# Optimization experiments

Hardware: AMD Instinct MI355X
Metric: run time of the kernel (lower is better)

## Reference

```python
import jax, jax.numpy as jnp
import numpy as np

C = 768; NH = 12; HD = 64; WS = 14; VPT = 10; H0 = 64; B = 8
SCALE = HD ** -0.5


def layernorm(x, w, b, eps=1e-5):
    m = x.mean(-1, keepdims=True)
    v = x.var(-1, keepdims=True)
    return (x - m) / jnp.sqrt(v + eps) * w + b


def setup_inputs() -> dict:
    key = jax.random.key(0)
    ks = jax.random.split(key, 8)
    def rn(k, shape, s=0.02):
        return jax.random.normal(k, shape, jnp.float32) * s
    L = VPT + H0 * H0
    return {
        "x": jax.random.normal(ks[0], (B, L, C), jnp.float32),
        "ln1_w": jnp.ones((C,), jnp.float32),
        "ln1_b": jnp.zeros((C,), jnp.float32),
        "qkv_w": rn(ks[1], (3 * C, C)),
        "qkv_b": jnp.zeros((3 * C,), jnp.float32),
        "proj_w": rn(ks[2], (C, C)),
        "proj_b": jnp.zeros((C,), jnp.float32),
        "rel_pos_h": rn(ks[3], (2 * WS - 1, HD)),
        "rel_pos_w": rn(ks[4], (2 * WS - 1, HD)),
        "ln2_w": jnp.ones((C,), jnp.float32),
        "ln2_b": jnp.zeros((C,), jnp.float32),
        "mlp_w1": rn(ks[5], (4 * C, C)),
        "mlp_b1": jnp.zeros((4 * C,), jnp.float32),
        "mlp_w2": rn(ks[6], (C, 4 * C)),
        "mlp_b2": jnp.zeros((C,), jnp.float32),
        "H": H0,
        "W": H0,
    }


def reference(x, ln1_w, ln1_b, qkv_w, qkv_b, proj_w, proj_b, rel_pos_h, rel_pos_w,
              ln2_w, ln2_b, mlp_w1, mlp_b1, mlp_w2, mlp_b2, H, W):
    B_, L, C_ = x.shape
    shortcut = x
    xn = layernorm(x, ln1_w, ln1_b)

    # --- window partition (SAM style, pad bottom/right) ---
    prompt = xn[:, :VPT]                           # (B, VPT, C)
    sp = xn[:, VPT:].reshape(B_, H, W, C_)
    pad_h = (WS - H % WS) % WS
    pad_w = (WS - W % WS) % WS
    Hp, Wp = H + pad_h, W + pad_w
    sp = jnp.pad(sp, ((0, 0), (0, pad_h), (0, pad_w), (0, 0)))
    nh, nw = Hp // WS, Wp // WS
    win = sp.reshape(B_, nh, WS, nw, WS, C_).transpose(0, 1, 3, 2, 4, 5)
    win = win.reshape(-1, WS * WS, C_)             # (B*nwin, WS*WS, C), batch-major
    nwin = nh * nw
    # faithful to original: prompts broadcast window-major, windows are batch-major
    pr = jnp.broadcast_to(prompt[None], (nwin, B_, VPT, C_)).reshape(-1, VPT, C_)
    tok = jnp.concatenate([pr, win], axis=1)       # (Bw, Lw, C)
    Bw, Lw, _ = tok.shape

    # --- attention with decomposed rel-pos ---
    qkv = tok @ qkv_w.T + qkv_b
    qkv = qkv.reshape(Bw, Lw, 3, NH, HD).transpose(2, 0, 3, 1, 4).reshape(3, Bw * NH, Lw, HD)
    q, k, v = qkv[0], qkv[1], qkv[2]
    attn = (q * SCALE) @ k.transpose(0, 2, 1)      # (Bw*NH, Lw, Lw)

    coords = jnp.arange(WS)[:, None] - jnp.arange(WS)[None, :] + (WS - 1)
    Rh = rel_pos_h[coords]                         # (WS, WS, HD)
    Rw = rel_pos_w[coords]
    rq = q[:, VPT:].reshape(Bw * NH, WS, WS, HD)
    rel_h = jnp.einsum('bhwc,hkc->bhwk', rq, Rh)
    rel_w = jnp.einsum('bhwc,wkc->bhwk', rq, Rw)
    ori = attn[:, VPT:, VPT:].reshape(-1, WS, WS, WS, WS)
    ori = ori + rel_h[:, :, :, :, None] + rel_w[:, :, :, None, :]
    attn = attn.at[:, VPT:, VPT:].set(ori.reshape(-1, WS * WS, WS * WS))

    attn = jax.nn.softmax(attn, axis=-1)
    out = (attn @ v).reshape(Bw, NH, Lw, HD).transpose(0, 2, 1, 3).reshape(Bw, Lw, C_)
    out = out @ proj_w.T + proj_b

    # --- window unpartition ---
    pr_out = out[:, :VPT].reshape(nwin, B_, VPT, C_).mean(0)   # (B, VPT, C)
    wo = out[:, VPT:].reshape(B_, nh, nw, WS, WS, C_).transpose(0, 1, 3, 2, 4, 5)
    wo = wo.reshape(B_, Hp, Wp, C_)[:, :H, :W].reshape(B_, H * W, C_)
    x2 = jnp.concatenate([pr_out, wo], axis=1)

    x2 = shortcut + x2
    h = layernorm(x2, ln2_w, ln2_b)
    h = jax.nn.gelu(h @ mlp_w1.T + mlp_b1, approximate=False)
    x2 = x2 + (h @ mlp_w2.T + mlp_b2)
    return x2
```

## Files before the change

### kernel.cpp

```cpp
#include <hip/hip_runtime.h>
#include <hip/hip_fp16.h>

#define Bb 8
#define Ll 4106
#define Cc 768
#define VPT_ 10
#define WSz 14
#define NWIN 25
#define BW_ 200
#define LW_ 206
#define NHh 12
#define HDd 64

typedef _Float16 half8 __attribute__((ext_vector_type(8)));
typedef float floatx4 __attribute__((ext_vector_type(4)));

__device__ __forceinline__ void gload16(const _Float16* g, _Float16* l) {
    __builtin_amdgcn_global_load_lds(
        (const __attribute__((address_space(1))) void*)g,
        (__attribute__((address_space(3))) void*)l, 16, 0, 0);
}

__global__ void f2h_kernel(const float* __restrict__ in, _Float16* __restrict__ out, int n) {
    int i = blockIdx.x * 256 + threadIdx.x;
    if (i < n) out[i] = (_Float16)in[i];
}

__global__ __launch_bounds__(256) void ln1_scatter_kernel(
    const float* __restrict__ x, const float* __restrict__ w, const float* __restrict__ bia,
    _Float16* __restrict__ tok)
{
    int r = blockIdx.x;
    int b = r / Ll, l = r % Ll;
    const float* xr = x + (size_t)r * Cc;
    int t = threadIdx.x;
    float v0 = xr[t], v1 = xr[t + 256], v2 = xr[t + 512];
    float s1 = v0 + v1 + v2;
    float s2 = v0 * v0 + v1 * v1 + v2 * v2;
    #pragma unroll
    for (int off = 32; off > 0; off >>= 1) {
        s1 += __shfl_down(s1, off);
        s2 += __shfl_down(s2, off);
    }
    __shared__ float red[8];
    int wv = t >> 6, ln = t & 63;
    if (ln == 0) { red[wv] = s1; red[4 + wv] = s2; }
    __syncthreads();
    float fs1 = red[0] + red[1] + red[2] + red[3];
    float fs2 = red[4] + red[5] + red[6] + red[7];
    float mean = fs1 * (1.0f / Cc);
    float var  = fs2 * (1.0f / Cc) - mean * mean;
    float rstd = rsqrtf(var + 1e-5f);
    float vv[3] = {v0, v1, v2};
    if (l < VPT_) {
        #pragma unroll
        for (int i = 0; i < 3; ++i) {
            int c = t + i * 256;
            _Float16 hy = (_Float16)((vv[i] - mean) * rstd * w[c] + bia[c]);
            for (int wi = 0; wi < NWIN; ++wi)
                tok[((size_t)(wi * Bb + b) * LW_ + l) * Cc + c] = hy;
        }
    } else {
        int sidx = l - VPT_;
        int ii = sidx >> 6, jj = sidx & 63;
        size_t drow = (size_t)(b * NWIN + (ii / WSz) * 5 + (jj / WSz)) * LW_
                      + VPT_ + (ii % WSz) * WSz + (jj % WSz);
        #pragma unroll
        for (int i = 0; i < 3; ++i) {
            int c = t + i * 256;
            tok[drow * Cc + c] = (_Float16)((vv[i] - mean) * rstd * w[c] + bia[c]);
        }
    }
}

__global__ __launch_bounds__(256) void ln2_kernel(
    const _Float16* __restrict__ x2, const float* __restrict__ w, const float* __restrict__ bia,
    _Float16* __restrict__ xn)
{
    int r = blockIdx.x;
    const _Float16* xr = x2 + (size_t)r * Cc;
    int t = threadIdx.x;
    float v0 = (float)xr[t], v1 = (float)xr[t + 256], v2 = (float)xr[t + 512];
    float s1 = v0 + v1 + v2;
    float s2 = v0 * v0 + v1 * v1 + v2 * v2;
    #pragma unroll
    for (int off = 32; off > 0; off >>= 1) {
        s1 += __shfl_down(s1, off);
        s2 += __shfl_down(s2, off);
    }
    __shared__ float red[8];
    int wv = t >> 6, ln = t & 63;
    if (ln == 0) { red[wv] = s1; red[4 + wv] = s2; }
    __syncthreads();
    float fs1 = red[0] + red[1] + red[2] + red[3];
    float fs2 = red[4] + red[5] + red[6] + red[7];
    float mean = fs1 * (1.0f / Cc);
    float var  = fs2 * (1.0f / Cc) - mean * mean;
    float rstd = rsqrtf(var + 1e-5f);
    float vv[3] = {v0, v1, v2};
    #pragma unroll
    for (int i = 0; i < 3; ++i) {
        int c = t + i * 256;
        xn[(size_t)r * Cc + c] = (_Float16)((vv[i] - mean) * rstd * w[c] + bia[c]);
    }
}

template <int EPI>
__global__ __launch_bounds__(256) void gemm128(
    const _Float16* __restrict__ A, const _Float16* __restrict__ W,
    const float* __restrict__ bias, const _Float16* __restrict__ addsrc,
    _Float16* __restrict__ outH, float* __restrict__ outF,
    int M, int N, int K, int gm, int gn)
{
    __shared__ alignas(16) _Float16 As[128 * 32];
    __shared__ alignas(16) _Float16 Bs[128 * 32];

    int pid = blockIdx.x;
    int width = 8 * gn;
    int gid = pid / width;
    int first = gid * 8;
    int gsz = gm - first; if (gsz > 8) gsz = 8;
    int rem = pid - gid * width;
    int pm = first + rem % gsz;
    int pn = rem / gsz;
    int row0 = pm * 128, col0 = pn * 128;

    int tid = threadIdx.x;
    int wv = tid >> 6, ln = tid & 63;
    int n = ln & 15, quad = ln >> 4;
    int wr = wv >> 1, wc = wv & 1;
    int lr = ln >> 2, lg = ln & 3;

    int lsw = (lg ^ ((lr >> 1) & 3)) * 8;
    int ar0 = row0 + wv * 16 + lr;        if (ar0 > M - 1) ar0 = M - 1;
    int ar1 = row0 + (wv + 4) * 16 + lr;  if (ar1 > M - 1) ar1 = M - 1;
    const _Float16* Ap0 = A + (size_t)ar0 * K + lsw;
    const _Float16* Ap1 = A + (size_t)ar1 * K + lsw;
    const _Float16* Bp0 = W + (size_t)(col0 + wv * 16 + lr) * K + lsw;
    const _Float16* Bp1 = W + (size_t)(col0 + (wv + 4) * 16 + lr) * K + lsw;
    _Float16* lA0 = As + wv * 512;
    _Float16* lA1 = As + (wv + 4) * 512;
    _Float16* lB0 = Bs + wv * 512;
    _Float16* lB1 = Bs + (wv + 4) * 512;

    const int cq = (quad ^ ((n >> 1) & 3)) * 8;

    floatx4 acc[4][4] = {};

    for (int k0 = 0; k0 < K; k0 += 32) {
        __syncthreads();
        gload16(Ap0 + k0, lA0);
        gload16(Ap1 + k0, lA1);
        gload16(Bp0 + k0, lB0);
        gload16(Bp1 + k0, lB1);
        __syncthreads();
        half8 af[4], bf[4];
        #pragma unroll
        for (int i = 0; i < 4; ++i)
            af[i] = *reinterpret_cast<const half8*>(&As[(wr * 64 + i * 16 + n) * 32 + cq]);
        #pragma unroll
        for (int j = 0; j < 4; ++j)
            bf[j] = *reinterpret_cast<const half8*>(&Bs[(wc * 64 + j * 16 + n) * 32 + cq]);
        #pragma unroll
        for (int i = 0; i < 4; ++i)
            #pragma unroll
            for (int j = 0; j < 4; ++j)
                acc[i][j] = __builtin_amdgcn_mfma_f32_16x16x32_f16(af[i], bf[j], acc[i][j], 0, 0, 0);
    }

    float bv[4];
    #pragma unroll
    for (int j = 0; j < 4; ++j) bv[j] = bias[col0 + wc * 64 + j * 16 + n];

    if (EPI == 2) {
        #pragma unroll
        for (int i = 0; i < 4; ++i)
            #pragma unroll
            for (int j = 0; j < 4; ++j) {
                int col = col0 + wc * 64 + j * 16 + n;
                #pragma unroll
                for (int rr = 0; rr < 4; ++rr) {
                    int row = row0 + wr * 64 + i * 16 + quad * 4 + rr;
                    if (row < M) {
                        size_t off = (size_t)row * N + col;
                        outF[off] = acc[i][j][rr] + bv[j] + (float)addsrc[off];
                    }
                }
            }
    } else {
        __syncthreads();
        _Float16* Tb = (wv < 2 ? As : Bs) + (wv & 1) * 2048;
        #pragma unroll
        for (int i = 0; i < 4; ++i) {
            #pragma unroll
            for (int j = 0; j < 4; ++j)
                #pragma unroll
                for (int rr = 0; rr < 4; ++rr) {
                    float v = acc[i][j][rr] + bv[j];
                    if (EPI == 1) v = 0.5f * v * (1.0f + erff(v * 0.70710678118654752f));
                    Tb[(quad * 4 + rr) * 72 + j * 16 + n] = (_Float16)v;
                }
            __syncthreads();
            int row = row0 + wr * 64 + i * 16 + lr;
            if (row < M) {
                uint4 p0 = *reinterpret_cast<const uint4*>(&Tb[lr * 72 + lg * 8]);
                uint4 p1 = *reinterpret_cast<const uint4*>(&Tb[lr * 72 + 32 + lg * 8]);
                _Float16* po = outH + (size_t)row * N + col0 + wc * 64 + lg * 8;
                *reinterpret_cast<uint4*>(po) = p0;
                *reinterpret_cast<uint4*>(po + 32) = p1;
            }
        }
    }
}

__global__ __launch_bounds__(256, 2) void attn_mfma_kernel(
    const _Float16* __restrict__ qkv,
    const float* __restrict__ relh, const float* __restrict__ relw,
    _Float16* __restrict__ attout)
{
    __shared__ alignas(16) _Float16 Ks[208 * 72];
    __shared__ alignas(16) _Float16 Vt[64 * 232];
    __shared__ alignas(16) _Float16 Pc[4][16 * 40];
    __shared__ alignas(16) float    Tabs[4][896];
    const int bwi = blockIdx.x / NHh, hh = blockIdx.x % NHh;
    const int tid = threadIdx.x;
    const _Float16* base = qkv + (size_t)bwi * LW_ * 2304 + hh * HDd;

    const int wv = tid >> 6, ln = tid & 63;
    const int n = ln & 15, quad = ln >> 4;

    half8 qa0, qa1;
    {
        int qrow = wv * 16 + n; if (qrow > 205) qrow = 205;
        const _Float16* qp = base + (size_t)qrow * 2304 + quad * 8;
        qa0 = *reinterpret_cast<const half8*>(qp);
        qa1 = *reinterpret_cast<const half8*>(qp + 32);
    }

    for (int idx = tid; idx < LW_ * 8; idx += 256) {
        int row = idx >> 3, c8 = idx & 7;
        *reinterpret_cast<uint4*>(&Ks[row * 72 + c8 * 8]) =
            *reinterpret_cast<const uint4*>(base + (size_t)row * 2304 + 768 + c8 * 8);
    }
    for (int idx = tid; idx < LW_ * 64; idx += 256) {
        int row = idx >> 6, d = idx & 63;
        Vt[d * 232 + row] = base[(size_t)row * 2304 + 1536 + d];
    }
    for (int idx = tid; idx < 64 * 26; idx += 256) {
        int d = idx / 26, c = idx - d * 26;
        Vt[d * 232 + 206 + c] = (_Float16)0.0f;
    }

    half8 bh[2][2], bwf[2][2];
    #pragma unroll
    for (int ct = 0; ct < 2; ++ct) {
        int j = ct * 16 + n; if (j > 26) j = 26;
        #pragma unroll
        for (int kk = 0; kk < 2; ++kk) {
            const float* ph = relh + j * 64 + kk * 32 + quad * 8;
            const float* pw = relw + j * 64 + kk * 32 + quad * 8;
            half8 hf, wf;
            #pragma unroll
            for (int e = 0; e < 8; ++e) { hf[e] = (_Float16)ph[e]; wf[e] = (_Float16)pw[e]; }
            bh[ct][kk] = hf; bwf[ct][kk] = wf;
        }
    }

    int khv[13], kwv[13];
    #pragma unroll
    for (int ct = 0; ct < 13; ++ct) {
        int key = ct * 16 + n;
        int k2 = key - VPT_; if (k2 < 0) k2 = 0;
        khv[ct] = k2 / WSz; kwv[ct] = k2 - khv[ct] * WSz;
    }
    __syncthreads();

    float* tw_t = Tabs[wv];
    float* th_t = Tabs[wv] + 448;
    _Float16* pcw = &Pc[wv][0];

    for (int rt = wv; rt < 13; rt += 4) {
        int nrt = rt + 4; if (nrt > 12) nrt = 12;
        int nqrow = nrt * 16 + n; if (nqrow > 205) nqrow = 205;
        const _Float16* nqp = base + (size_t)nqrow * 2304 + quad * 8;
        half8 nq0 = *reinterpret_cast<const half8*>(nqp);
        half8 nq1 = *reinterpret_cast<const half8*>(nqp + 32);

        floatx4 th0 = {}, th1 = {}, tw0 = {}, tw1 = {};
        th0 = __builtin_amdgcn_mfma_f32_16x16x32_f16(qa0, bh[0][0], th0, 0, 0, 0);
        th0 = __builtin_amdgcn_mfma_f32_16x16x32_f16(qa1, bh[0][1], th0, 0, 0, 0);
        th1 = __builtin_amdgcn_mfma_f32_16x16x32_f16(qa0, bh[1][0], th1, 0, 0, 0);
        th1 = __builtin_amdgcn_mfma_f32_16x16x32_f16(qa1, bh[1][1], th1, 0, 0, 0);
        tw0 = __builtin_amdgcn_mfma_f32_16x16x32_f16(qa0, bwf[0][0], tw0, 0, 0, 0);
        tw0 = __builtin_amdgcn_mfma_f32_16x16x32_f16(qa1, bwf[0][1], tw0, 0, 0, 0);
        tw1 = __builtin_amdgcn_mfma_f32_16x16x32_f16(qa0, bwf[1][0], tw1, 0, 0, 0);
        tw1 = __builtin_amdgcn_mfma_f32_16x16x32_f16(qa1, bwf[1][1], tw1, 0, 0, 0);

        #pragma unroll
        for (int rr = 0; rr < 4; ++rr) {
            int lrow = quad * 4 + rr;
            th_t[lrow * 28 + n] = th0[rr];
            tw_t[lrow * 28 + n] = tw0[rr];
            if (n < 12) {
                th_t[lrow * 28 + 16 + n] = th1[rr];
                tw_t[lrow * 28 + 16 + n] = tw1[rr];
            }
        }

        floatx4 s[13];
        #pragma unroll
        for (int ct = 0; ct < 13; ++ct) {
            half8 kb0 = *reinterpret_cast<const half8*>(&Ks[(ct * 16 + n) * 72 + quad * 8]);
            half8 kb1 = *reinterpret_cast<const half8*>(&Ks[(ct * 16 + n) * 72 + 32 + quad * 8]);
            floatx4 a = {};
            a = __builtin_amdgcn_mfma_f32_16x16x32_f16(qa0, kb0, a, 0, 0, 0);
            a = __builtin_amdgcn_mfma_f32_16x16x32_f16(qa1, kb1, a, 0, 0, 0);
            s[ct] = a;
        }

        #pragma unroll
        for (int rr = 0; rr < 4; ++rr) {
            int row = rt * 16 + quad * 4 + rr;
            bool rowok = (row >= VPT_) && (row < LW_);
            int q2 = row - VPT_; if (q2 < 0) q2 = 0;
            int qh = q2 / WSz, qw = q2 - qh * WSz;
            const float* thr = th_t + (quad * 4 + rr) * 28;
            const float* twr = tw_t + (quad * 4 + rr) * 28;
            #pragma unroll
            for (int ct = 0; ct < 13; ++ct) {
                int key = ct * 16 + n;
                float tv = thr[qh - khv[ct] + 13] + twr[qw - kwv[ct] + 13];
                float sv = s[ct][rr] * 0.125f;
                sv += (rowok && key >= VPT_ && key < LW_) ? tv : 0.0f;
                if (key >= LW_) sv = -1e30f;
                s[ct][rr] = sv;
            }
        }

        float mx[4] = {-1e30f, -1e30f, -1e30f, -1e30f};
        #pragma unroll
        for (int ct = 0; ct < 13; ++ct)
            #pragma unroll
            for (int rr = 0; rr < 4; ++rr) mx[rr] = fmaxf(mx[rr], s[ct][rr]);
        #pragma unroll
        for (int rr = 0; rr < 4; ++rr)
            #pragma unroll
            for (int off = 1; off < 16; off <<= 1) mx[rr] = fmaxf(mx[rr], __shfl_xor(mx[rr], off));
        float sm[4] = {0.f, 0.f, 0.f, 0.f};
        #pragma unroll
        for (int ct = 0; ct < 13; ++ct)
            #pragma unroll
            for (int rr = 0; rr < 4; ++rr) {
                float p = __expf(s[ct][rr] - mx[rr]);
                s[ct][rr] = p; sm[rr] += p;
            }
        #pragma unroll
        for (int rr = 0; rr < 4; ++rr) {
            #pragma unroll
            for (int off = 1; off < 16; off <<= 1) sm[rr] += __shfl_xor(sm[rr], off);
            sm[rr] = 1.0f / sm[rr];
        }
        #pragma unroll
        for (int ct = 0; ct < 13; ++ct)
            #pragma unroll
            for (int rr = 0; rr < 4; ++rr) s[ct][rr] *= sm[rr];

        floatx4 o[4] = {};
        #pragma unroll
        for (int kt = 0; kt < 7; ++kt) {
            #pragma unroll
            for (int h2 = 0; h2 < 2; ++h2) {
                int ct = kt * 2 + h2;
                #pragma unroll
                for (int rr = 0; rr < 4; ++rr) {
                    float pv = (ct < 13) ? s[ct][rr] : 0.0f;
                    pcw[(quad * 4 + rr) * 40 + h2 * 16 + n] = (_Float16)pv;
                }
            }
            half8 pa = *reinterpret_cast<const half8*>(&pcw[n * 40 + quad * 8]);
            #pragma unroll
            for (int dt = 0; dt < 4; ++dt) {
                half8 vb = *reinterpret_cast<const half8*>(&Vt[(dt * 16 + n) * 232 + kt * 32 + quad * 8]);
                o[dt] = __builtin_amdgcn_mfma_f32_16x16x32_f16(pa, vb, o[dt], 0, 0, 0);
            }
        }

        #pragma unroll
        for (int dt = 0; dt < 4; ++dt)
            #pragma unroll
            for (int rr = 0; rr < 4; ++rr) {
                int row = rt * 16 + quad * 4 + rr;
                if (row < LW_)
                    attout[((size_t)(bwi * LW_ + row)) * Cc + hh * HDd + dt * 16 + n] = (_Float16)o[dt][rr];
            }

        qa0 = nq0; qa1 = nq1;
    }
}

__global__ __launch_bounds__(256) void build_x2_kernel(
    const float* __restrict__ x, const _Float16* __restrict__ proj, _Float16* __restrict__ x2)
{
    int r = blockIdx.x;
    int b = r / Ll, l = r % Ll;
    int t = threadIdx.x;
    size_t srow = 0;
    bool prompt = (l < VPT_);
    if (!prompt) {
        int sidx = l - VPT_;
        int ii = sidx >> 6, jj = sidx & 63;
        srow = (size_t)(b * NWIN + (ii / WSz) * 5 + (jj / WSz)) * LW_
               + VPT_ + (ii % WSz) * WSz + (jj % WSz);
    }
    #pragma unroll
    for (int i = 0; i < 3; ++i) {
        int c = t + i * 256;
        float v;
        if (prompt) {
            float s = 0.0f;
            for (int wi = 0; wi < NWIN; ++wi)
                s += (float)proj[((size_t)(wi * Bb + b) * LW_ + l) * Cc + c];
            v = s * (1.0f / NWIN);
        } else {
            v = (float)proj[srow * Cc + c];
        }
        size_t off = (size_t)r * Cc + c;
        x2[off] = (_Float16)(x[off] + v);
    }
}

extern "C" void kernel_launch(void* const* d_in, const int* in_sizes, int n_in,
                              void* d_out, int out_size, void* d_ws, size_t ws_size,
                              hipStream_t stream)
{
    const float* x     = (const float*)d_in[0];
    const float* ln1w  = (const float*)d_in[1];
    const float* ln1b  = (const float*)d_in[2];
    const float* qkvw  = (const float*)d_in[3];
    const float* qkvb  = (const float*)d_in[4];
    const float* projw = (const float*)d_in[5];
    const float* projb = (const float*)d_in[6];
    const float* relh  = (const float*)d_in[7];
    const float* relw  = (const float*)d_in[8];
    const float* ln2w  = (const float*)d_in[9];
    const float* ln2b  = (const float*)d_in[10];
    const float* w1    = (const float*)d_in[11];
    const float* b1    = (const float*)d_in[12];
    const float* w2    = (const float*)d_in[13];
    const float* b2    = (const float*)d_in[14];
    float* out = (float*)d_out;
    char* ws = (char*)d_ws;

    _Float16* wqkv_h  = (_Float16*)(ws + 0);
    _Float16* wproj_h = (_Float16*)(ws + 3538944);
    _Float16* w1_h    = (_Float16*)(ws + 4718592);
    _Float16* w2_h    = (_Float16*)(ws + 9437184);
    _Float16* tokA    = (_Float16*)(ws + 14155776);
    char* regB = ws + 77438976;
    _Float16* qkv_h  = (_Float16*)regB;
    _Float16* proj_h = (_Float16*)regB;
    _Float16* hbuf   = (_Float16*)regB;
    _Float16* x2h    = (_Float16*)(regB + 100909056);

    f2h_kernel<<<(2304 * 768 + 255) / 256, 256, 0, stream>>>(qkvw, wqkv_h, 2304 * 768);
    f2h_kernel<<<(768 * 768 + 255) / 256, 256, 0, stream>>>(projw, wproj_h, 768 * 768);
    f2h_kernel<<<(3072 * 768 + 255) / 256, 256, 0, stream>>>(w1, w1_h, 3072 * 768);
    f2h_kernel<<<(768 * 3072 + 255) / 256, 256, 0, stream>>>(w2, w2_h, 768 * 3072);
    hipMemsetAsync(tokA, 0, (size_t)41200 * 768 * 2, stream);
    ln1_scatter_kernel<<<Bb * Ll, 256, 0, stream>>>(x, ln1w, ln1b, tokA);
    gemm128<0><<<322 * 18, 256, 0, stream>>>(tokA, wqkv_h, qkvb, nullptr, qkv_h, nullptr,
                                             41200, 2304, 768, 322, 18);
    attn_mfma_kernel<<<BW_ * NHh, 256, 0, stream>>>(qkv_h, relh, relw, tokA);
    gemm128<0><<<322 * 6, 256, 0, stream>>>(tokA, wproj_h, projb, nullptr, proj_h, nullptr,
                                            41200, 768, 768, 322, 6);
    build_x2_kernel<<<Bb * Ll, 256, 0, stream>>>(x, proj_h, x2h);
    ln2_kernel<<<Bb * Ll, 256, 0, stream>>>(x2h, ln2w, ln2b, tokA);
    for (int ch = 0; ch < 2; ++ch) {
        size_t r0 = (size_t)ch * 16424;
        gemm128<1><<<129 * 24, 256, 0, stream>>>(tokA + r0 * 768, w1_h, b1, nullptr, hbuf, nullptr,
                                                 16424, 3072, 768, 129, 24);
        gemm128<2><<<129 * 6, 256, 0, stream>>>(hbuf, w2_h, b2, x2h + r0 * 768, nullptr, out + r0 * 768,
                                                16424, 768, 3072, 129, 6);
    }
}
```

Measured before the change: 1.398 ms.

## Run QKV and proj GEMMs on unpadded tokens and gather windows inside attention

```diff
diff --git a/kernel.cpp b/kernel.cpp
--- a/kernel.cpp
+++ b/kernel.cpp
@@ -26,12 +26,11 @@
     if (i < n) out[i] = (_Float16)in[i];
 }
 
-__global__ __launch_bounds__(256) void ln1_scatter_kernel(
+__global__ __launch_bounds__(256) void ln1_kernel(
     const float* __restrict__ x, const float* __restrict__ w, const float* __restrict__ bia,
-    _Float16* __restrict__ tok)
+    _Float16* __restrict__ xn)
 {
     int r = blockIdx.x;
-    int b = r / Ll, l = r % Ll;
     const float* xr = x + (size_t)r * Cc;
     int t = threadIdx.x;
     float v0 = xr[t], v1 = xr[t + 256], v2 = xr[t + 512];
@@ -52,24 +51,10 @@
     float var  = fs2 * (1.0f / Cc) - mean * mean;
     float rstd = rsqrtf(var + 1e-5f);
     float vv[3] = {v0, v1, v2};
-    if (l < VPT_) {
-        #pragma unroll
-        for (int i = 0; i < 3; ++i) {
-            int c = t + i * 256;
-            _Float16 hy = (_Float16)((vv[i] - mean) * rstd * w[c] + bia[c]);
-            for (int wi = 0; wi < NWIN; ++wi)
-                tok[((size_t)(wi * Bb + b) * LW_ + l) * Cc + c] = hy;
-        }
-    } else {
-        int sidx = l - VPT_;
-        int ii = sidx >> 6, jj = sidx & 63;
-        size_t drow = (size_t)(b * NWIN + (ii / WSz) * 5 + (jj / WSz)) * LW_
-                      + VPT_ + (ii % WSz) * WSz + (jj % WSz);
-        #pragma unroll
-        for (int i = 0; i < 3; ++i) {
-            int c = t + i * 256;
-            tok[drow * Cc + c] = (_Float16)((vv[i] - mean) * rstd * w[c] + bia[c]);
-        }
+    #pragma unroll
+    for (int i = 0; i < 3; ++i) {
+        int c = t + i * 256;
+        xn[(size_t)r * Cc + c] = (_Float16)((vv[i] - mean) * rstd * w[c] + bia[c]);
     }
 }
 
@@ -105,10 +90,27 @@
     }
 }
 
+__global__ __launch_bounds__(256) void pmean_kernel(
+    const _Float16* __restrict__ attP, _Float16* __restrict__ attS)
+{
+    int r = blockIdx.x;
+    int b = r / VPT_, l = r % VPT_;
+    int t = threadIdx.x;
+    #pragma unroll
+    for (int i = 0; i < 3; ++i) {
+        int c = t + i * 256;
+        float s = 0.0f;
+        for (int wi = 0; wi < NWIN; ++wi)
+            s += (float)attP[((size_t)((wi * Bb + b) * VPT_ + l)) * Cc + c];
+        attS[((size_t)(b * Ll + l)) * Cc + c] = (_Float16)(s * (1.0f / NWIN));
+    }
+}
+
 template <int EPI>
 __global__ __launch_bounds__(256) void gemm128(
     const _Float16* __restrict__ A, const _Float16* __restrict__ W,
     const float* __restrict__ bias, const _Float16* __restrict__ addsrc,
+    const float* __restrict__ addF,
     _Float16* __restrict__ outH, float* __restrict__ outF,
     int M, int N, int K, int gm, int gn)
 {
@@ -184,6 +186,21 @@
                     if (row < M) {
                         size_t off = (size_t)row * N + col;
                         outF[off] = acc[i][j][rr] + bv[j] + (float)addsrc[off];
+                    }
+                }
+            }
+    } else if (EPI == 3) {
+        #pragma unroll
+        for (int i = 0; i < 4; ++i)
+            #pragma unroll
+            for (int j = 0; j < 4; ++j) {
+                int col = col0 + wc * 64 + j * 16 + n;
+                #pragma unroll
+                for (int rr = 0; rr < 4; ++rr) {
+                    int row = row0 + wr * 64 + i * 16 + quad * 4 + rr;
+                    if (row < M) {
+                        size_t off = (size_t)row * N + col;
+                        outH[off] = (_Float16)(acc[i][j][rr] + bv[j] + addF[off]);
                     }
                 }
             }
@@ -214,41 +231,36 @@
 }
 
 __global__ __launch_bounds__(256, 2) void attn_mfma_kernel(
-    const _Float16* __restrict__ qkv,
+    const _Float16* __restrict__ qkv, const _Float16* __restrict__ qkvbh,
     const float* __restrict__ relh, const float* __restrict__ relw,
-    _Float16* __restrict__ attout)
+    _Float16* __restrict__ attS, _Float16* __restrict__ attP)
 {
     __shared__ alignas(16) _Float16 Ks[208 * 72];
     __shared__ alignas(16) _Float16 Vt[64 * 232];
     __shared__ alignas(16) _Float16 Pc[4][16 * 40];
     __shared__ alignas(16) float    Tabs[4][896];
+    __shared__ int rowOff[208];
     const int bwi = blockIdx.x / NHh, hh = blockIdx.x % NHh;
     const int tid = threadIdx.x;
-    const _Float16* base = qkv + (size_t)bwi * LW_ * 2304 + hh * HDd;
+
+    const int bp = bwi & 7;
+    const int bs = bwi / NWIN;
+    const int wis = bwi % NWIN;
+    const int wh = wis / 5, ww = wis % 5;
 
     const int wv = tid >> 6, ln = tid & 63;
     const int n = ln & 15, quad = ln >> 4;
 
-    half8 qa0, qa1;
-    {
-        int qrow = wv * 16 + n; if (qrow > 205) qrow = 205;
-        const _Float16* qp = base + (size_t)qrow * 2304 + quad * 8;
-        qa0 = *reinterpret_cast<const half8*>(qp);
-        qa1 = *reinterpret_cast<const half8*>(qp + 32);
-    }
-
-    for (int idx = tid; idx < LW_ * 8; idx += 256) {
-        int row = idx >> 3, c8 = idx & 7;
-        *reinterpret_cast<uint4*>(&Ks[row * 72 + c8 * 8]) =
-            *reinterpret_cast<const uint4*>(base + (size_t)row * 2304 + 768 + c8 * 8);
-    }
-    for (int idx = tid; idx < LW_ * 64; idx += 256) {
-        int row = idx >> 6, d = idx & 63;
-        Vt[d * 232 + row] = base[(size_t)row * 2304 + 1536 + d];
-    }
-    for (int idx = tid; idx < 64 * 26; idx += 256) {
-        int d = idx / 26, c = idx - d * 26;
-        Vt[d * 232 + 206 + c] = (_Float16)0.0f;
+    if (tid < 208) {
+        int row = tid, off = -1;
+        if (row < VPT_) off = bp * Ll + row;
+        else if (row < LW_) {
+            int s = row - VPT_;
+            int i = s / WSz, j = s - i * WSz;
+            int gi = wh * WSz + i, gj = ww * WSz + j;
+            if (gi < 64 && gj < 64) off = bs * Ll + VPT_ + gi * 64 + gj;
+        }
+        rowOff[row] = off;
     }
 
     half8 bh[2][2], bwf[2][2];
@@ -275,6 +287,34 @@
     }
     __syncthreads();
 
+    half8 qa0, qa1;
+    {
+        int qrow = wv * 16 + n; if (qrow > 205) qrow = 205;
+        int ro = rowOff[qrow];
+        const _Float16* qp = (ro >= 0 ? qkv + (size_t)ro * 2304 : qkvbh) + hh * HDd + quad * 8;
+        qa0 = *reinterpret_cast<const half8*>(qp);
+        qa1 = *reinterpret_cast<const half8*>(qp + 32);
+    }
+
+    for (int idx = tid; idx < LW_ * 8; idx += 256) {
+        int row = idx >> 3, c8 = idx & 7;
+        int ro = rowOff[row];
+        const _Float16* src = (ro >= 0 ? qkv + (size_t)ro * 2304 : qkvbh) + 768 + hh * HDd;
+        *reinterpret_cast<uint4*>(&Ks[row * 72 + c8 * 8]) =
+            *reinterpret_cast<const uint4*>(src + c8 * 8);
+    }
+    for (int idx = tid; idx < LW_ * 64; idx += 256) {
+        int row = idx >> 6, d = idx & 63;
+        int ro = rowOff[row];
+        const _Float16* src = (ro >= 0 ? qkv + (size_t)ro * 2304 : qkvbh) + 1536 + hh * HDd;
+        Vt[d * 232 + row] = src[d];
+    }
+    for (int idx = tid; idx < 64 * 26; idx += 256) {
+        int d = idx / 26, c = idx - d * 26;
+        Vt[d * 232 + 206 + c] = (_Float16)0.0f;
+    }
+    __syncthreads();
+
     float* tw_t = Tabs[wv];
     float* th_t = Tabs[wv] + 448;
     _Float16* pcw = &Pc[wv][0];
@@ -282,7 +322,8 @@
     for (int rt = wv; rt < 13; rt += 4) {
         int nrt = rt + 4; if (nrt > 12) nrt = 12;
         int nqrow = nrt * 16 + n; if (nqrow > 205) nqrow = 205;
-        const _Float16* nqp = base + (size_t)nqrow * 2304 + quad * 8;
+        int nro = rowOff[nqrow];
+        const _Float16* nqp = (nro >= 0 ? qkv + (size_t)nro * 2304 : qkvbh) + hh * HDd + quad * 8;
         half8 nq0 = *reinterpret_cast<const half8*>(nqp);
         half8 nq1 = *reinterpret_cast<const half8*>(nqp + 32);
 
@@ -390,42 +431,18 @@
             #pragma unroll
             for (int rr = 0; rr < 4; ++rr) {
                 int row = rt * 16 + quad * 4 + rr;
-                if (row < LW_)
-                    attout[((size_t)(bwi * LW_ + row)) * Cc + hh * HDd + dt * 16 + n] = (_Float16)o[dt][rr];
+                if (row >= LW_) continue;
+                _Float16 val = (_Float16)o[dt][rr];
+                int col = hh * HDd + dt * 16 + n;
+                if (row < VPT_) {
+                    attP[((size_t)(bwi * VPT_ + row)) * Cc + col] = val;
+                } else {
+                    int g = rowOff[row];
+                    if (g >= 0) attS[(size_t)g * Cc + col] = val;
+                }
             }
 
         qa0 = nq0; qa1 = nq1;
-    }
-}
-
-__global__ __launch_bounds__(256) void build_x2_kernel(
-    const float* __restrict__ x, const _Float16* __restrict__ proj, _Float16* __restrict__ x2)
-{
-    int r = blockIdx.x;
-    int b = r / Ll, l = r % Ll;
-    int t = threadIdx.x;
-    size_t srow = 0;
-    bool prompt = (l < VPT_);
-    if (!prompt) {
-        int sidx = l - VPT_;
-        int ii = sidx >> 6, jj = sidx & 63;
-        srow = (size_t)(b * NWIN + (ii / WSz) * 5 + (jj / WSz)) * LW_
-               + VPT_ + (ii % WSz) * WSz + (jj % WSz);
-    }
-    #pragma unroll
-    for (int i = 0; i < 3; ++i) {
-        int c = t + i * 256;
-        float v;
-        if (prompt) {
-            float s = 0.0f;
-            for (int wi = 0; wi < NWIN; ++wi)
-                s += (float)proj[((size_t)(wi * Bb + b) * LW_ + l) * Cc + c];
-            v = s * (1.0f / NWIN);
-        } else {
-            v = (float)proj[srow * Cc + c];
-        }
-        size_t off = (size_t)r * Cc + c;
-        x2[off] = (_Float16)(x[off] + v);
     }
 }
 
@@ -455,10 +472,11 @@
     _Float16* wproj_h = (_Float16*)(ws + 3538944);
     _Float16* w1_h    = (_Float16*)(ws + 4718592);
     _Float16* w2_h    = (_Float16*)(ws + 9437184);
-    _Float16* tokA    = (_Float16*)(ws + 14155776);
+    _Float16* qkvb_h  = (_Float16*)(ws + 14155776);
+    _Float16* attP    = (_Float16*)(ws + 14160384);
+    _Float16* tokA    = (_Float16*)(ws + 17232384);
     char* regB = ws + 77438976;
     _Float16* qkv_h  = (_Float16*)regB;
-    _Float16* proj_h = (_Float16*)regB;
     _Float16* hbuf   = (_Float16*)regB;
     _Float16* x2h    = (_Float16*)(regB + 100909056);
 
@@ -466,20 +484,20 @@
     f2h_kernel<<<(768 * 768 + 255) / 256, 256, 0, stream>>>(projw, wproj_h, 768 * 768);
     f2h_kernel<<<(3072 * 768 + 255) / 256, 256, 0, stream>>>(w1, w1_h, 3072 * 768);
     f2h_kernel<<<(768 * 3072 + 255) / 256, 256, 0, stream>>>(w2, w2_h, 768 * 3072);
-    hipMemsetAsync(tokA, 0, (size_t)41200 * 768 * 2, stream);
-    ln1_scatter_kernel<<<Bb * Ll, 256, 0, stream>>>(x, ln1w, ln1b, tokA);
-    gemm128<0><<<322 * 18, 256, 0, stream>>>(tokA, wqkv_h, qkvb, nullptr, qkv_h, nullptr,
-                                             41200, 2304, 768, 322, 18);
-    attn_mfma_kernel<<<BW_ * NHh, 256, 0, stream>>>(qkv_h, relh, relw, tokA);
-    gemm128<0><<<322 * 6, 256, 0, stream>>>(tokA, wproj_h, projb, nullptr, proj_h, nullptr,
-                                            41200, 768, 768, 322, 6);
-    build_x2_kernel<<<Bb * Ll, 256, 0, stream>>>(x, proj_h, x2h);
+    f2h_kernel<<<9, 256, 0, stream>>>(qkvb, qkvb_h, 2304);
+    ln1_kernel<<<Bb * Ll, 256, 0, stream>>>(x, ln1w, ln1b, tokA);
+    gemm128<0><<<257 * 18, 256, 0, stream>>>(tokA, wqkv_h, qkvb, nullptr, nullptr, qkv_h, nullptr,
+                                             32848, 2304, 768, 257, 18);
+    attn_mfma_kernel<<<BW_ * NHh, 256, 0, stream>>>(qkv_h, qkvb_h, relh, relw, tokA, attP);
+    pmean_kernel<<<Bb * VPT_, 256, 0, stream>>>(attP, tokA);
+    gemm128<3><<<257 * 6, 256, 0, stream>>>(tokA, wproj_h, projb, nullptr, x, x2h, nullptr,
+                                            32848, 768, 768, 257, 6);
     ln2_kernel<<<Bb * Ll, 256, 0, stream>>>(x2h, ln2w, ln2b, tokA);
     for (int ch = 0; ch < 2; ++ch) {
         size_t r0 = (size_t)ch * 16424;
-        gemm128<1><<<129 * 24, 256, 0, stream>>>(tokA + r0 * 768, w1_h, b1, nullptr, hbuf, nullptr,
+        gemm128<1><<<129 * 24, 256, 0, stream>>>(tokA + r0 * 768, w1_h, b1, nullptr, nullptr, hbuf, nullptr,
                                                  16424, 3072, 768, 129, 24);
-        gemm128<2><<<129 * 6, 256, 0, stream>>>(hbuf, w2_h, b2, x2h + r0 * 768, nullptr, out + r0 * 768,
+        gemm128<2><<<129 * 6, 256, 0, stream>>>(hbuf, w2_h, b2, x2h + r0 * 768, nullptr, nullptr, out + r0 * 768,
                                                 16424, 768, 3072, 129, 6);
     }
 }
```

Result: no change. 1.402 ms (+0.3%).
